# Optimization experiments

Hardware: AMD Instinct MI355X
Metric: run time of the kernel (lower is better)

## Reference

```python
import math
import jax, jax.numpy as jnp
import numpy as np

B, S, D = 8, 920, 1536
H, HD = 4, 384            # num heads, head dim; all_head = H*HD = 1536
MAX_POS = 920
L = 2 * MAX_POS - 1       # 1839 relative positions


def setup_inputs() -> dict:
    key = jax.random.key(0)
    k1, k2, k3, k4, k5 = jax.random.split(key, 5)
    return {
        "hidden_states": jax.random.normal(k1, (B, S, D), dtype=jnp.float32),
        "w_query": jax.random.normal(k2, (D, H * HD), dtype=jnp.float32) * 0.02,
        "w_key": jax.random.normal(k3, (D, H * HD), dtype=jnp.float32) * 0.02,
        "w_value": jax.random.normal(k4, (D, H * HD), dtype=jnp.float32) * 0.02,
        "distance_embedding": jax.random.normal(k5, (L, HD), dtype=jnp.float32) * 0.02,
    }


def reshape_fortran(x, shape):
    # Matches torch reference: reverse-permute, C reshape of reversed shape, reverse-permute back.
    x = jnp.transpose(x, tuple(reversed(range(x.ndim))))
    x = jnp.reshape(x, tuple(reversed(shape)))
    return jnp.transpose(x, tuple(reversed(range(len(shape)))))


def relative_position_embedding_rotate(scores):
    # scores: [B, H, L, S]
    scores = jnp.transpose(scores, (0, 2, 3, 1))  # [B, L, S, H]
    b, hs, s, h = scores.shape
    scores = jnp.concatenate([scores, jnp.zeros((b, s, s, h), scores.dtype)], axis=1)
    scores = reshape_fortran(scores, [b, (hs + s) * s, 1, h])
    scores = scores[:, : (s + hs - 1) * s]
    scores = reshape_fortran(scores, [b, hs + s - 1, s, h])
    halfpoint = hs // 2
    scores = scores[:, halfpoint : halfpoint + s]          # [B, S, S, H]
    scores = jnp.transpose(scores, (0, 2, 1, 3))           # transpose(1,2)
    return jnp.transpose(scores, (0, 3, 1, 2))             # [B, H, S, S]


def reference(hidden_states, w_query, w_key, w_value, distance_embedding):
    inv = 1.0 / math.sqrt(HD)
    q = (hidden_states @ w_query) * inv                    # [B, S, H*HD]
    k = hidden_states @ w_key
    v = hidden_states @ w_value

    def heads(x):  # [B,S,H*HD] -> [B,H,S,HD]
        return jnp.transpose(x.reshape(B, S, H, HD), (0, 2, 1, 3))

    q, k, v = heads(q), heads(k), heads(v)

    scores = jnp.einsum("bhqd,bhkd->bhqk", q, k)           # [B,H,S,S]
    rel = jnp.einsum("ld,bhsd->bhls", distance_embedding, q)  # [B,H,L,S]
    scores = scores + relative_position_embedding_rotate(rel)

    probs = jax.nn.softmax(scores, axis=-1)
    ctx = jnp.einsum("bhqk,bhkd->bhqd", probs, v)          # [B,H,S,HD]
    ctx = jnp.transpose(ctx, (0, 2, 1, 3)).reshape(B, S, H * HD)
    return ctx
```

## Files before the change

### kernel.cpp

```cpp
#include <hip/hip_runtime.h>

#define S_LEN 920
#define DMODEL 1536
#define NH 4
#define HD 384
#define LREL 1839
#define BATCH 8
#define MTOT (BATCH * S_LEN)
#define KPAD 960
#define NBH (BATCH * NH)

#define CHS   5652480UL
#define BSLAB 2826240UL
#define KOFF  1413120UL

#define EB_BYTES 1412352UL
#define VT_BYTES 23592960UL

typedef __attribute__((ext_vector_type(8))) short  s16x8;
typedef __attribute__((ext_vector_type(4))) short  s16x4;
typedef __attribute__((ext_vector_type(8))) __bf16 bf16x8;
typedef __attribute__((ext_vector_type(4))) float  f32x4;

__device__ __forceinline__ short f2b(float x) {
  unsigned u = __builtin_bit_cast(unsigned, x);
  unsigned r = (u + 0x7FFFu + ((u >> 16) & 1u)) >> 16;
  return (short)r;
}
__device__ __forceinline__ float b2f(short s) {
  unsigned u = ((unsigned)(unsigned short)s) << 16;
  return __builtin_bit_cast(float, u);
}

__device__ __forceinline__ void load_lds16(const short* g, short* lds) {
  __builtin_amdgcn_global_load_lds(
      (const __attribute__((address_space(1))) void*)g,
      (__attribute__((address_space(3))) void*)lds, 16, 0, 0);
}

__device__ __forceinline__ f32x4 mfma_bf16(s16x8 a, s16x8 b, f32x4 c) {
  return __builtin_amdgcn_mfma_f32_16x16x32_bf16(
      __builtin_bit_cast(bf16x8, a), __builtin_bit_cast(bf16x8, b), c, 0, 0, 0);
}

__device__ __forceinline__ s16x8 frag_swz(const short* base, int row, int kk, int lq) {
  int byte = (row << 7) + (kk << 6) + (lq << 4);
  byte ^= (row & 7) << 4;
  return *(const s16x8*)((const char*)base + byte);
}

template <int NT>
__device__ __forceinline__ void gemm_pipe(short* smem,
    const short* __restrict__ A, int ldA, int mClamp, int m0,
    const short* __restrict__ B, int ldB, int nClamp, int n0,
    f32x4 acc[4][6]) {
  short* const A0 = smem;
  short* const B0 = smem + 16384;
  short* const A1 = smem + 28672;
  short* const B1 = smem + 45056;

  const int tid = threadIdx.x, w = tid >> 6, lane = tid & 63;
  const int lr = lane & 15, lq = lane >> 4;
  const int wr = w >> 1, wc = w & 1;

  const short* pa[4]; int la[4];
  const short* pb[3]; int lb[3];
  {
    const int rl = lane >> 3, c = lane & 7;
#pragma unroll
    for (int i = 0; i < 4; ++i) {
      int r = w * 32 + i * 8 + rl;
      int ra = m0 + r; if (ra > mClamp) ra = mClamp;
      pa[i] = A + (size_t)ra * ldA + ((c ^ (r & 7)) * 8);
      la[i] = (w * 32 + i * 8) * 64;
    }
#pragma unroll
    for (int i = 0; i < 3; ++i) {
      int r = w * 24 + i * 8 + rl;
      int rb = n0 + r; if (rb > nClamp) rb = nClamp;
      pb[i] = B + (size_t)rb * ldB + ((c ^ (r & 7)) * 8);
      lb[i] = (w * 24 + i * 8) * 64;
    }
  }

#pragma unroll
  for (int i = 0; i < 4; ++i)
#pragma unroll
    for (int j = 0; j < 6; ++j) acc[i][j] = (f32x4){0.f, 0.f, 0.f, 0.f};

#pragma unroll
  for (int i = 0; i < 4; ++i) load_lds16(pa[i], A0 + la[i]);
#pragma unroll
  for (int i = 0; i < 3; ++i) load_lds16(pb[i], B0 + lb[i]);

  for (int kt = 0; kt < NT; ++kt) {
    short* const Ab = (kt & 1) ? A1 : A0;
    short* const Bb = (kt & 1) ? B1 : B0;
    short* const An = (kt & 1) ? A0 : A1;
    short* const Bn = (kt & 1) ? B0 : B1;

    if (kt + 1 < NT) {
      const int k0 = (kt + 1) * 64;
#pragma unroll
      for (int i = 0; i < 4; ++i) load_lds16(pa[i] + k0, An + la[i]);
#pragma unroll
      for (int i = 0; i < 3; ++i) load_lds16(pb[i] + k0, Bn + lb[i]);
      asm volatile("s_waitcnt vmcnt(7)" ::: "memory");
    } else {
      asm volatile("s_waitcnt vmcnt(0)" ::: "memory");
    }
    __builtin_amdgcn_sched_barrier(0);
    __builtin_amdgcn_s_barrier();
    __builtin_amdgcn_sched_barrier(0);

    s16x8 a[4], bb[3];
#pragma unroll
    for (int f = 0; f < 4; ++f) a[f] = frag_swz(Ab, wr * 64 + f * 16 + lr, 0, lq);
#pragma unroll
    for (int f = 0; f < 3; ++f) bb[f] = frag_swz(Bb, wc * 96 + f * 16 + lr, 0, lq);
    __builtin_amdgcn_s_barrier();
    __builtin_amdgcn_s_setprio(1);
#pragma unroll
    for (int i = 0; i < 4; ++i)
#pragma unroll
      for (int j = 0; j < 3; ++j) acc[i][j] = mfma_bf16(a[i], bb[j], acc[i][j]);
    __builtin_amdgcn_s_setprio(0);
    __builtin_amdgcn_s_barrier();
#pragma unroll
    for (int f = 0; f < 3; ++f) bb[f] = frag_swz(Bb, wc * 96 + (3 + f) * 16 + lr, 0, lq);
    __builtin_amdgcn_s_barrier();
    __builtin_amdgcn_s_setprio(1);
#pragma unroll
    for (int i = 0; i < 4; ++i)
#pragma unroll
      for (int j = 0; j < 3; ++j) acc[i][3 + j] = mfma_bf16(a[i], bb[j], acc[i][3 + j]);
    __builtin_amdgcn_s_setprio(0);
    __builtin_amdgcn_s_barrier();
#pragma unroll
    for (int f = 0; f < 4; ++f) a[f] = frag_swz(Ab, wr * 64 + f * 16 + lr, 1, lq);
#pragma unroll
    for (int f = 0; f < 3; ++f) bb[f] = frag_swz(Bb, wc * 96 + f * 16 + lr, 1, lq);
    __builtin_amdgcn_s_barrier();
    __builtin_amdgcn_s_setprio(1);
#pragma unroll
    for (int i = 0; i < 4; ++i)
#pragma unroll
      for (int j = 0; j < 3; ++j) acc[i][j] = mfma_bf16(a[i], bb[j], acc[i][j]);
    __builtin_amdgcn_s_setprio(0);
    __builtin_amdgcn_s_barrier();
#pragma unroll
    for (int f = 0; f < 3; ++f) bb[f] = frag_swz(Bb, wc * 96 + (3 + f) * 16 + lr, 1, lq);
    __builtin_amdgcn_s_barrier();
    __builtin_amdgcn_s_setprio(1);
#pragma unroll
    for (int i = 0; i < 4; ++i)
#pragma unroll
      for (int j = 0; j < 3; ++j) acc[i][3 + j] = mfma_bf16(a[i], bb[j], acc[i][3 + j]);
    __builtin_amdgcn_s_setprio(0);
    __builtin_amdgcn_s_barrier();
  }
}

__global__ void k_cast(const float* __restrict__ X, short* __restrict__ O, int n4) {
  int i = blockIdx.x * blockDim.x + threadIdx.x;
  if (i >= n4) return;
  float4 v = ((const float4*)X)[i];
  s16x4 o = {f2b(v.x), f2b(v.y), f2b(v.z), f2b(v.w)};
  *(s16x4*)&O[(size_t)i * 4] = o;
}

#define EB_N4   (LREL * HD / 4)
#define PAD_N   (NBH * HD * (KPAD - S_LEN))
__global__ void k_prep_ev(const float* __restrict__ de, short* __restrict__ Eb,
                          short* __restrict__ Vt) {
  int i = blockIdx.x * blockDim.x + threadIdx.x;
  if (i < EB_N4) {
    float4 v = ((const float4*)de)[i];
    s16x4 o = {f2b(v.x), f2b(v.y), f2b(v.z), f2b(v.w)};
    *(s16x4*)&Eb[(size_t)i * 4] = o;
  } else {
    int idx = i - EB_N4;
    if (idx < PAD_N) {
      int bhd = idx / (KPAD - S_LEN);
      int s = S_LEN + idx - bhd * (KPAD - S_LEN);
      Vt[(size_t)bhd * KPAD + s] = 0;
    }
  }
}

__global__ void k_transpose_w(const float* __restrict__ W0, const float* __restrict__ W1,
                              const float* __restrict__ W2, short* __restrict__ Wt) {
  const float* W = (blockIdx.z == 0) ? W0 : ((blockIdx.z == 1) ? W1 : W2);
  short* O = Wt + (size_t)blockIdx.z * DMODEL * DMODEL;
  __shared__ float t[32][33];
  int tx = threadIdx.x, ty = threadIdx.y;
  int n0 = blockIdx.x * 32, k0 = blockIdx.y * 32;
#pragma unroll
  for (int i = 0; i < 4; ++i)
    t[ty + i * 8][tx] = W[(size_t)(k0 + ty + i * 8) * DMODEL + n0 + tx];
  __syncthreads();
#pragma unroll
  for (int i = 0; i < 4; ++i)
    O[(size_t)(n0 + ty + i * 8) * DMODEL + k0 + tx] = f2b(t[tx][ty + i * 8]);
}

#define QKV_NT (DMODEL / 64)

__global__ __launch_bounds__(512, 2) void k_gemm_qkv(const short* __restrict__ Xb,
                                                     const short* __restrict__ Wt,
                                                     short* __restrict__ out16,
                                                     short* __restrict__ Vt) {
  __shared__ short smem[57344];
  const int z = blockIdx.z;
  const int t = blockIdx.x;
  const int t2 = (t & 7) * 29 + (t >> 3);
  const int m0 = (t2 >> 3) * 256;
  const int n0 = (t2 & 7) * 192;

  const int tid = threadIdx.x, w = tid >> 6, lane = tid & 63;
  const int lr = lane & 15, lq = lane >> 4;
  const int wr = w >> 1, wc = w & 1;

  f32x4 acc[4][6];
  gemm_pipe<QKV_NT>(smem, Xb, DMODEL, MTOT - 1, m0,
                    Wt + (size_t)z * DMODEL * DMODEL, DMODEL, DMODEL - 1, n0, acc);

  __syncthreads();
  const float inv = 0.05103103630798287f;
  if (z != 2) {
    short* T = smem;
#pragma unroll
    for (int i = 0; i < 4; ++i)
#pragma unroll
      for (int j = 0; j < 6; ++j) {
        int ml = wr * 64 + i * 16 + lq * 4;
        int nl = wc * 96 + j * 16 + lr;
#pragma unroll
        for (int r = 0; r < 4; ++r) {
          float v = acc[i][j][r];
          T[(ml + r) * 200 + nl] = f2b(z == 0 ? v * inv : v);
        }
      }
    __syncthreads();
    for (int u = 0; u < 12; ++u) {
      int unit = u * 512 + tid;
      int ml = unit / 24, c = unit - ml * 24;
      int m = m0 + ml;
      if (m < MTOT) {
        int b = m / S_LEN, s = m - b * S_LEN;
        short* dst = out16 + (size_t)(b >> 1) * CHS + (size_t)(b & 1) * BSLAB +
                     (z == 1 ? KOFF : 0UL) + (size_t)s * DMODEL + n0 + c * 8;
        *(s16x8*)dst = *(const s16x8*)&T[ml * 200 + c * 8];
      }
    }
  } else {
    short* T = smem;
#pragma unroll
    for (int i = 0; i < 4; ++i)
#pragma unroll
      for (int j = 0; j < 6; ++j) {
        int ml = wr * 64 + i * 16 + lq * 4;
        int nl = wc * 96 + j * 16 + lr;
#pragma unroll
        for (int r = 0; r < 4; ++r)
          T[nl * 264 + ml + r] = f2b(acc[i][j][r]);
      }
    __syncthreads();
    const int h = n0 / HD;
    const int d0 = n0 - h * HD;
    for (int u = 0; u < 12; ++u) {
      int unit = u * 512 + tid;
      int nl = unit >> 5, c = unit & 31;
      int m = m0 + c * 8;
      if (m < MTOT) {
        int b = m / S_LEN, s = m - b * S_LEN;
        size_t row = (size_t)(b * NH + h) * HD + d0 + nl;
        *(s16x8*)&Vt[row * KPAD + s] = *(const s16x8*)&T[nl * 264 + c * 8];
      }
    }
  }
}

#define FKV 192
#define FNT 5

#define WAITVM(N) { asm volatile("s_waitcnt vmcnt(" #N ")" ::: "memory"); \
  __builtin_amdgcn_sched_barrier(0); __builtin_amdgcn_s_barrier(); \
  __builtin_amdgcn_sched_barrier(0); }

#define LBAR { asm volatile("s_waitcnt lgkmcnt(0)" ::: "memory"); \
  __builtin_amdgcn_sched_barrier(0); __builtin_amdgcn_s_barrier(); \
  __builtin_amdgcn_sched_barrier(0); }

#define NOISSUE { }

#define STAGE_E(BUF, C, L0) { \
  _Pragma("unroll") for (int i_ = 0; i_ < 4; ++i_) { \
    int r_ = w * 32 + i_ * 8 + rl; \
    int rg_ = (L0) + r_; rg_ = rg_ < 0 ? 0 : (rg_ > LREL - 1 ? LREL - 1 : rg_); \
    load_lds16(Eb + (size_t)rg_ * HD + ((cs ^ (r_ & 7)) * 8) + (C) * 64, \
               (BUF) + (w * 32 + i_ * 8) * 64); } }

#define STAGE_K(BUF, C) { \
  _Pragma("unroll") for (int i_ = 0; i_ < 3; ++i_) { \
    int r_ = w * 24 + i_ * 8 + rl; \
    int rg_ = kv0 + r_; if (rg_ > S_LEN - 1) rg_ = S_LEN - 1; \
    load_lds16(Kp + (size_t)rg_ * DMODEL + ((cs ^ (r_ & 7)) * 8) + (C) * 64, \
               (BUF) + (w * 24 + i_ * 8) * 64); } }

#define STAGE_V(BUF, HF, SC) { \
  _Pragma("unroll") for (int i_ = 0; i_ < 3; ++i_) { \
    int r_ = w * 24 + i_ * 8 + rl; \
    load_lds16(Vb + (size_t)((HF) * 192 + r_) * KPAD + kv0 + (SC) * 64 + ((cs ^ (r_ & 7)) * 8), \
               (BUF) + (w * 24 + i_ * 8) * 64); } }

#define GSLOT_T(CUR, C, ISSUE, WVM) { ISSUE; WVM; \
  s16x8 a_[2][2], b_[2][4]; \
  _Pragma("unroll") for (int k_ = 0; k_ < 2; ++k_) { \
    _Pragma("unroll") for (int i_ = 0; i_ < 2; ++i_) \
      a_[i_][k_] = frag_swz(QL + (C) * 4096, wm * 32 + i_ * 16 + lr, k_, lq); \
    _Pragma("unroll") for (int j_ = 0; j_ < 4; ++j_) \
      b_[k_][j_] = frag_swz((CUR), wn * 64 + j_ * 16 + lr, k_, lq); } \
  __builtin_amdgcn_s_setprio(1); \
  _Pragma("unroll") for (int k_ = 0; k_ < 2; ++k_) \
    _Pragma("unroll") for (int i_ = 0; i_ < 2; ++i_) \
      _Pragma("unroll") for (int j_ = 0; j_ < 4; ++j_) \
        acc_t[i_][j_] = mfma_bf16(a_[i_][k_], b_[k_][j_], acc_t[i_][j_]); \
  __builtin_amdgcn_s_setprio(0); __builtin_amdgcn_s_barrier(); }

#define GSLOT_S(CUR, C, ISSUE, WVM) { ISSUE; WVM; \
  s16x8 a_[2][2], b_[2][3]; \
  _Pragma("unroll") for (int k_ = 0; k_ < 2; ++k_) { \
    _Pragma("unroll") for (int i_ = 0; i_ < 2; ++i_) \
      a_[i_][k_] = frag_swz(QL + (C) * 4096, wm * 32 + i_ * 16 + lr, k_, lq); \
    _Pragma("unroll") for (int j_ = 0; j_ < 3; ++j_) \
      b_[k_][j_] = frag_swz((CUR), wn * 48 + j_ * 16 + lr, k_, lq); } \
  __builtin_amdgcn_s_setprio(1); \
  _Pragma("unroll") for (int k_ = 0; k_ < 2; ++k_) \
    _Pragma("unroll") for (int i_ = 0; i_ < 2; ++i_) \
      _Pragma("unroll") for (int j_ = 0; j_ < 3; ++j_) \
        acc_s[i_][j_] = mfma_bf16(a_[i_][k_], b_[k_][j_], acc_s[i_][j_]); \
  __builtin_amdgcn_s_setprio(0); __builtin_amdgcn_s_barrier(); }

#define GSLOT_PV(CUR, SC, HF, ISSUE, WVM) { ISSUE; WVM; \
  s16x8 a_[2][2], b_[2][3]; \
  _Pragma("unroll") for (int k_ = 0; k_ < 2; ++k_) { \
    _Pragma("unroll") for (int i_ = 0; i_ < 2; ++i_) \
      a_[i_][k_] = frag_swz(TLP + (SC) * 4096, wm * 32 + i_ * 16 + lr, k_, lq); \
    _Pragma("unroll") for (int j_ = 0; j_ < 3; ++j_) \
      b_[k_][j_] = frag_swz((CUR), wn * 48 + j_ * 16 + lr, k_, lq); } \
  __builtin_amdgcn_s_setprio(1); \
  _Pragma("unroll") for (int k_ = 0; k_ < 2; ++k_) \
    _Pragma("unroll") for (int i_ = 0; i_ < 2; ++i_) \
      _Pragma("unroll") for (int j_ = 0; j_ < 3; ++j_) \
        acc_o[i_][(HF) * 3 + j_] = mfma_bf16(a_[i_][k_], b_[k_][j_], acc_o[i_][(HF) * 3 + j_]); \
  __builtin_amdgcn_s_setprio(0); __builtin_amdgcn_s_barrier(); }

__global__ __launch_bounds__(512, 1) void k_fused(const short* __restrict__ out16,
                                                  const short* __restrict__ Vt,
                                                  const short* __restrict__ Eb,
                                                  float* __restrict__ O, int half) {
  __shared__ short smem[74752];
  short* const QL  = smem;
  short* const B0  = smem + 24576;
  short* const B1  = smem + 40960;
  short* const TLP = smem + 57344;
  float* const pmax = (float*)(smem + 73728);
  float* const psum = pmax + 256;

  const int f  = blockIdx.x;
  const int f2 = (f & 7) * 30 + (f >> 3);
  const int mt = f2 % 15, bhl = f2 / 15;
  const int bh = half * 16 + bhl, b = bh >> 2, h = bh & 3;
  const int m0 = mt * 64;

  const int tid = threadIdx.x, w = tid >> 6, lane = tid & 63;
  const int lr = lane & 15, lq = lane >> 4;
  const int wm = w >> 2, wn = w & 3;
  const int rl = lane >> 3, cs = lane & 7;

  const short* Qp = out16 + (size_t)(b >> 1) * CHS + (size_t)(b & 1) * BSLAB + h * HD;
  const short* Kp = Qp + KOFF;
  const short* Vb = Vt + (size_t)bh * HD * KPAD;
  float* Ob = O + (size_t)bhl * S_LEN * HD;

  f32x4 acc_o[2][6];
  float Mst[2][4], Lst[2][4];
#pragma unroll
  for (int i = 0; i < 2; ++i) {
#pragma unroll
    for (int j = 0; j < 6; ++j) acc_o[i][j] = (f32x4){0.f, 0.f, 0.f, 0.f};
#pragma unroll
    for (int r = 0; r < 4; ++r) { Mst[i][r] = -1e30f; Lst[i][r] = 0.f; }
  }

#pragma unroll
  for (int i = 0; i < 6; ++i) {
    int rq = w * 8 + rl;
    int rg = m0 + rq; if (rg > S_LEN - 1) rg = S_LEN - 1;
    load_lds16(Qp + (size_t)rg * DMODEL + ((cs ^ (rq & 7)) * 8) + i * 64,
               QL + i * 4096 + (w * 8) * 64);
  }
  { const int l0p = 856 - m0; STAGE_E(B0, 0, l0p); }

  for (int t = 0; t < FNT; ++t) {
    const int kv0 = t * FKV;
    const int l0 = kv0 - m0 + 856;

    f32x4 acc_t[2][4];
#pragma unroll
    for (int i = 0; i < 2; ++i)
#pragma unroll
      for (int j = 0; j < 4; ++j) acc_t[i][j] = (f32x4){0.f, 0.f, 0.f, 0.f};

    GSLOT_T(B0, 0, STAGE_E(B1, 1, l0), WAITVM(4));
    GSLOT_T(B1, 1, STAGE_E(B0, 2, l0), WAITVM(4));
    GSLOT_T(B0, 2, STAGE_E(B1, 3, l0), WAITVM(4));
    GSLOT_T(B1, 3, STAGE_E(B0, 4, l0), WAITVM(4));
    GSLOT_T(B0, 4, STAGE_E(B1, 5, l0), WAITVM(4));
    GSLOT_T(B1, 5, STAGE_K(B0, 0),     WAITVM(3));

#pragma unroll
    for (int i = 0; i < 2; ++i)
#pragma unroll
      for (int j = 0; j < 4; ++j)
#pragma unroll
        for (int r = 0; r < 4; ++r) {
          int row = wm * 32 + i * 16 + lq * 4 + r;
          int col = wn * 64 + j * 16 + lr;
          TLP[row * 256 + col] = f2b(acc_t[i][j][r]);
        }
    LBAR;

    f32x4 acc_s[2][3];
#pragma unroll
    for (int i = 0; i < 2; ++i)
#pragma unroll
      for (int j = 0; j < 3; ++j) acc_s[i][j] = (f32x4){0.f, 0.f, 0.f, 0.f};

    GSLOT_S(B0, 0, STAGE_K(B1, 1), WAITVM(3));
    GSLOT_S(B1, 1, STAGE_K(B0, 2), WAITVM(3));
    GSLOT_S(B0, 2, STAGE_K(B1, 3), WAITVM(3));
    GSLOT_S(B1, 3, STAGE_K(B0, 4), WAITVM(3));
    GSLOT_S(B0, 4, STAGE_K(B1, 5), WAITVM(3));
    GSLOT_S(B1, 5, STAGE_V(B0, 0, 0), WAITVM(3));

#pragma unroll
    for (int i = 0; i < 2; ++i)
#pragma unroll
      for (int j = 0; j < 3; ++j) {
        int jpl = wn * 48 + j * 16 + lr;
        int jp = kv0 + jpl;
#pragma unroll
        for (int r = 0; r < 4; ++r) {
          int row = wm * 32 + i * 16 + lq * 4 + r;
          float x = acc_s[i][j][r] + b2f(TLP[row * 256 + (jpl - row + 63)]);
          acc_s[i][j][r] = (jp < S_LEN) ? x : -1e30f;
        }
      }
    {
      float tm[2][4];
#pragma unroll
      for (int i = 0; i < 2; ++i)
#pragma unroll
        for (int r = 0; r < 4; ++r) {
          float v = fmaxf(fmaxf(acc_s[i][0][r], acc_s[i][1][r]), acc_s[i][2][r]);
#pragma unroll
          for (int o = 1; o < 16; o <<= 1) v = fmaxf(v, __shfl_xor(v, o));
          tm[i][r] = v;
        }
      if (lr == 0) {
#pragma unroll
        for (int i = 0; i < 2; ++i)
#pragma unroll
          for (int r = 0; r < 4; ++r)
            pmax[wn * 64 + wm * 32 + i * 16 + lq * 4 + r] = tm[i][r];
      }
    }
    LBAR;
    float fexp[2][4], ps[2][4];
#pragma unroll
    for (int i = 0; i < 2; ++i)
#pragma unroll
      for (int r = 0; r < 4; ++r) {
        int row = wm * 32 + i * 16 + lq * 4 + r;
        float M2 = fmaxf(fmaxf(pmax[row], pmax[64 + row]),
                         fmaxf(pmax[128 + row], pmax[192 + row]));
        M2 = fmaxf(M2, Mst[i][r]);
        fexp[i][r] = __expf(Mst[i][r] - M2);
        Mst[i][r] = M2;
      }
#pragma unroll
    for (int i = 0; i < 2; ++i)
#pragma unroll
      for (int r = 0; r < 4; ++r) {
        float s0 = 0.f;
#pragma unroll
        for (int j = 0; j < 3; ++j) {
          float p = __expf(acc_s[i][j][r] - Mst[i][r]);
          acc_s[i][j][r] = p;
          s0 += p;
        }
#pragma unroll
        for (int o = 1; o < 16; o <<= 1) s0 += __shfl_xor(s0, o);
        ps[i][r] = s0;
#pragma unroll
        for (int jj = 0; jj < 6; ++jj) acc_o[i][jj][r] *= fexp[i][r];
      }
    if (lr == 0) {
#pragma unroll
      for (int i = 0; i < 2; ++i)
#pragma unroll
        for (int r = 0; r < 4; ++r)
          psum[wn * 64 + wm * 32 + i * 16 + lq * 4 + r] = ps[i][r];
    }
    LBAR;
#pragma unroll
    for (int i = 0; i < 2; ++i)
#pragma unroll
      for (int r = 0; r < 4; ++r) {
        int row = wm * 32 + i * 16 + lq * 4 + r;
        float ts = psum[row] + psum[64 + row] + psum[128 + row] + psum[192 + row];
        Lst[i][r] = Lst[i][r] * fexp[i][r] + ts;
      }
#pragma unroll
    for (int i = 0; i < 2; ++i)
#pragma unroll
      for (int j = 0; j < 3; ++j) {
        int c192 = wn * 48 + j * 16 + lr;
        int sc = c192 >> 6, c64 = c192 & 63;
#pragma unroll
        for (int r = 0; r < 4; ++r) {
          int row = wm * 32 + i * 16 + lq * 4 + r;
          int byte = sc * 8192 + row * 128 + ((c64 * 2) ^ ((row & 7) * 16));
          *(short*)((char*)TLP + byte) = f2b(acc_s[i][j][r]);
        }
      }
    LBAR;

    GSLOT_PV(B0, 0, 0, STAGE_V(B1, 0, 1), WAITVM(3));
    GSLOT_PV(B1, 1, 0, STAGE_V(B0, 0, 2), WAITVM(3));
    GSLOT_PV(B0, 2, 0, STAGE_V(B1, 1, 0), WAITVM(3));
    GSLOT_PV(B1, 0, 1, STAGE_V(B0, 1, 1), WAITVM(3));
    GSLOT_PV(B0, 1, 1, STAGE_V(B1, 1, 2), WAITVM(3));
    if (t < FNT - 1) {
      GSLOT_PV(B1, 2, 1, STAGE_E(B0, 0, l0 + FKV), WAITVM(4));
    } else {
      GSLOT_PV(B1, 2, 1, NOISSUE, WAITVM(0));
    }
  }

#pragma unroll
  for (int i = 0; i < 2; ++i)
#pragma unroll
    for (int r = 0; r < 4; ++r) {
      int m = m0 + wm * 32 + i * 16 + lq * 4 + r;
      if (m < S_LEN) {
        float rs = 1.0f / Lst[i][r];
#pragma unroll
        for (int jj = 0; jj < 6; ++jj) {
          int d = (jj / 3) * 192 + wn * 48 + (jj % 3) * 16 + lr;
          Ob[(size_t)m * HD + d] = acc_o[i][jj][r] * rs;
        }
      }
    }
}

__global__ __launch_bounds__(256) void k_copy_o(const float* __restrict__ O,
                                                float* __restrict__ out, int b0) {
  int i = blockIdx.x * 256 + threadIdx.x;
  if (i >= 16 * S_LEN * HD / 4) return;
  const int per_bh = S_LEN * HD / 4;
  int bhl = i / per_bh, rem = i - bhl * per_bh;
  int m = rem / (HD / 4), d4 = rem - m * (HD / 4);
  int b = b0 + (bhl >> 2), h = bhl & 3;
  float4 v = ((const float4*)O)[i];
  ((float4*)out)[((size_t)(b * S_LEN + m) * DMODEL + h * HD + d4 * 4) >> 2] = v;
}

extern "C" void kernel_launch(void* const* d_in, const int* in_sizes, int n_in,
                              void* d_out, int out_size, void* d_ws, size_t ws_size,
                              hipStream_t stream) {
  const float* hs = (const float*)d_in[0];
  const float* wq = (const float*)d_in[1];
  const float* wk = (const float*)d_in[2];
  const float* wv = (const float*)d_in[3];
  const float* de = (const float*)d_in[4];
  char* ws = (char*)d_ws;

  short* Xb = (short*)(ws + 0);
  short* Wt = (short*)(ws + 22609920UL);
  short* Eb = (short*)(ws + 36765696UL);
  short* Vt = (short*)(ws + 36765696UL + EB_BYTES);
  float* Og = (float*)(ws + 0);
  short* out16 = (short*)d_out;

  k_cast<<<(MTOT * DMODEL / 4 + 255) / 256, 256, 0, stream>>>(hs, Xb, MTOT * DMODEL / 4);
  k_prep_ev<<<(EB_N4 + PAD_N + 255) / 256, 256, 0, stream>>>(de, Eb, Vt);
  k_transpose_w<<<dim3(48, 48, 3), dim3(32, 8, 1), 0, stream>>>(wq, wk, wv, Wt);

  k_gemm_qkv<<<dim3(232, 1, 3), 512, 0, stream>>>(Xb, Wt, out16, Vt);

  for (int hf = 0; hf < 2; ++hf) {
    k_fused<<<dim3(240), 512, 0, stream>>>(out16, Vt, Eb, Og, hf);
    k_copy_o<<<dim3(5520), 256, 0, stream>>>(Og, (float*)d_out, hf * 4);
  }
}
```

Before: 423.5 us.

## Write attention output directly to final layout when workspace allows, single fused launch

When the workspace is large enough, Q and K are stored in dedicated workspace buffers instead of being packed into the output buffer. The fused attention kernel then writes its results straight to the final [B,S,H*HD] layout, and both halves run in one 480-block launch. This removes the intermediate O buffer, the two copy kernels and one launch boundary. It depends on ws_size, and the fallback path keeps the old two-pass scheme.

After: 414.9 us, median of 2. 1.02x faster.

```diff
diff --git a/kernel.cpp b/kernel.cpp
--- a/kernel.cpp
+++ b/kernel.cpp
@@ -16,6 +16,9 @@
 
 #define EB_BYTES 1412352UL
 #define VT_BYTES 23592960UL
+#define QW_OFF   61771008UL
+#define KW_OFF   84380928UL
+#define WS_DIRECT 106990848UL
 
 typedef __attribute__((ext_vector_type(8))) short  s16x8;
 typedef __attribute__((ext_vector_type(4))) short  s16x4;
@@ -209,7 +212,10 @@
 __global__ __launch_bounds__(512, 2) void k_gemm_qkv(const short* __restrict__ Xb,
                                                      const short* __restrict__ Wt,
                                                      short* __restrict__ out16,
-                                                     short* __restrict__ Vt) {
+                                                     short* __restrict__ Vt,
+                                                     short* __restrict__ Qw,
+                                                     short* __restrict__ Kw,
+                                                     int mode) {
   __shared__ short smem[57344];
   const int z = blockIdx.z;
   const int t = blockIdx.x;
@@ -247,9 +253,14 @@
       int ml = unit / 24, c = unit - ml * 24;
       int m = m0 + ml;
       if (m < MTOT) {
-        int b = m / S_LEN, s = m - b * S_LEN;
-        short* dst = out16 + (size_t)(b >> 1) * CHS + (size_t)(b & 1) * BSLAB +
-                     (z == 1 ? KOFF : 0UL) + (size_t)s * DMODEL + n0 + c * 8;
+        short* dst;
+        if (mode) {
+          dst = (z == 0 ? Qw : Kw) + (size_t)m * DMODEL + n0 + c * 8;
+        } else {
+          int b = m / S_LEN, s = m - b * S_LEN;
+          dst = out16 + (size_t)(b >> 1) * CHS + (size_t)(b & 1) * BSLAB +
+                (z == 1 ? KOFF : 0UL) + (size_t)s * DMODEL + n0 + c * 8;
+        }
         *(s16x8*)dst = *(const s16x8*)&T[ml * 200 + c * 8];
       }
     }
@@ -359,7 +370,10 @@
 __global__ __launch_bounds__(512, 1) void k_fused(const short* __restrict__ out16,
                                                   const short* __restrict__ Vt,
                                                   const short* __restrict__ Eb,
-                                                  float* __restrict__ O, int half) {
+                                                  float* __restrict__ O,
+                                                  const short* __restrict__ Qw,
+                                                  const short* __restrict__ Kw,
+                                                  int mode, int half) {
   __shared__ short smem[74752];
   short* const QL  = smem;
   short* const B0  = smem + 24576;
@@ -368,10 +382,12 @@
   float* const pmax = (float*)(smem + 73728);
   float* const psum = pmax + 256;
 
-  const int f  = blockIdx.x;
+  int f = blockIdx.x;
+  int hf = half;
+  if (hf < 0) { hf = (f >= 240) ? 1 : 0; if (hf) f -= 240; }
   const int f2 = (f & 7) * 30 + (f >> 3);
   const int mt = f2 % 15, bhl = f2 / 15;
-  const int bh = half * 16 + bhl, b = bh >> 2, h = bh & 3;
+  const int bh = hf * 16 + bhl, b = bh >> 2, h = bh & 3;
   const int m0 = mt * 64;
 
   const int tid = threadIdx.x, w = tid >> 6, lane = tid & 63;
@@ -379,10 +395,18 @@
   const int wm = w >> 2, wn = w & 3;
   const int rl = lane >> 3, cs = lane & 7;
 
-  const short* Qp = out16 + (size_t)(b >> 1) * CHS + (size_t)(b & 1) * BSLAB + h * HD;
-  const short* Kp = Qp + KOFF;
+  const short *Qp, *Kp;
+  if (mode) {
+    Qp = Qw + (size_t)b * S_LEN * DMODEL + h * HD;
+    Kp = Kw + (size_t)b * S_LEN * DMODEL + h * HD;
+  } else {
+    Qp = out16 + (size_t)(b >> 1) * CHS + (size_t)(b & 1) * BSLAB + h * HD;
+    Kp = Qp + KOFF;
+  }
   const short* Vb = Vt + (size_t)bh * HD * KPAD;
-  float* Ob = O + (size_t)bhl * S_LEN * HD;
+  float* const Obase = mode ? (O + (size_t)b * S_LEN * DMODEL + h * HD)
+                            : (O + (size_t)bhl * S_LEN * HD);
+  const int ostride = mode ? DMODEL : HD;
 
   f32x4 acc_o[2][6];
   float Mst[2][4], Lst[2][4];
@@ -560,7 +584,7 @@
 #pragma unroll
         for (int jj = 0; jj < 6; ++jj) {
           int d = (jj / 3) * 192 + wn * 48 + (jj % 3) * 16 + lr;
-          Ob[(size_t)m * HD + d] = acc_o[i][jj][r] * rs;
+          Obase[(size_t)m * ostride + d] = acc_o[i][jj][r] * rs;
         }
       }
     }
@@ -594,15 +618,24 @@
   short* Vt = (short*)(ws + 36765696UL + EB_BYTES);
   float* Og = (float*)(ws + 0);
   short* out16 = (short*)d_out;
+  const int direct = (ws_size >= WS_DIRECT) ? 1 : 0;
+  short* Qw = direct ? (short*)(ws + QW_OFF) : (short*)d_out;
+  short* Kw = direct ? (short*)(ws + KW_OFF) : (short*)d_out;
 
   k_cast<<<(MTOT * DMODEL / 4 + 255) / 256, 256, 0, stream>>>(hs, Xb, MTOT * DMODEL / 4);
   k_prep_ev<<<(EB_N4 + PAD_N + 255) / 256, 256, 0, stream>>>(de, Eb, Vt);
   k_transpose_w<<<dim3(48, 48, 3), dim3(32, 8, 1), 0, stream>>>(wq, wk, wv, Wt);
 
-  k_gemm_qkv<<<dim3(232, 1, 3), 512, 0, stream>>>(Xb, Wt, out16, Vt);
-
-  for (int hf = 0; hf < 2; ++hf) {
-    k_fused<<<dim3(240), 512, 0, stream>>>(out16, Vt, Eb, Og, hf);
-    k_copy_o<<<dim3(5520), 256, 0, stream>>>(Og, (float*)d_out, hf * 4);
-  }
-}
+  k_gemm_qkv<<<dim3(232, 1, 3), 512, 0, stream>>>(Xb, Wt, out16, Vt, Qw, Kw, direct);
+
+  if (direct) {
+    k_fused<<<dim3(480), 512, 0, stream>>>(out16, Vt, Eb, (float*)d_out,
+                                           Qw, Kw, 1, -1);
+  } else {
+    for (int hf = 0; hf < 2; ++hf) {
+      k_fused<<<dim3(240), 512, 0, stream>>>(out16, Vt, Eb, Og,
+                                             nullptr, nullptr, 0, hf);
+      k_copy_o<<<dim3(5520), 256, 0, stream>>>(Og, (float*)d_out, hf * 4);
+    }
+  }
+}
```
